# Optimization experiments

Hardware: AMD Instinct MI355X
Metric: run time of the kernel (lower is better)

The kernel has to match this reference:

```python
import jax, jax.numpy as jnp
import numpy as np

FREQ_DIM = 32
TIME_DIM = 32
HEADS = 8
TWO_PI = 6.283185307179586


def get_embeddings(B, H, W, freq_dim, time_dim, dtype):
    # freq embeddings over the height (frequency) axis
    nf = freq_dim // 2
    ln_x = jnp.log2(jnp.arange(0, H * nf, dtype=jnp.float32))
    ln_x = ln_x.at[0].set(-2.0)
    ln_x = ln_x.reshape(H, nf).T  # [nf, H]
    ln_x = ln_x * jnp.arange(1, nf + 1, dtype=jnp.float32)[:, None]
    # view_as_real(exp(1j*theta)) -> (cos, sin), interleaved per order along channel dim
    freq = jnp.stack([jnp.cos(ln_x), jnp.sin(ln_x)], axis=1).reshape(freq_dim, H)  # [freq_dim, H]
    freq = jnp.broadcast_to(freq[None, :, :, None], (B, freq_dim, H, W))

    # time embeddings over the width (time) axis
    nt = time_dim // 2
    k = jnp.arange(0, nt, dtype=jnp.float32) + 0.5  # [nt]
    x = jnp.arange(0, nt * W, dtype=jnp.float32).reshape(W, nt).T  # [nt, W]
    theta = k[:, None] * x / (W * nt) * TWO_PI  # [nt, W]
    time = jnp.stack([jnp.cos(theta), jnp.sin(theta)], axis=1).reshape(time_dim, W)  # [time_dim, W]
    time = jnp.broadcast_to(time[None, :, None, :], (B, time_dim, H, W))

    return jnp.concatenate([freq, time], axis=1).astype(dtype)  # [B, freq_dim+time_dim, H, W]


def setup_inputs() -> dict:
    key = jax.random.key(0)
    ks = jax.random.split(key, 6)
    B, C, H, W = 2, 512, 64, 32
    qkC = C + FREQ_DIM + TIME_DIM  # 576
    inner = HEADS * 64  # 512
    return {
        "hidden_states": jax.random.normal(ks[0], (B, C, H, W), dtype=jnp.float32),
        "Wq": jax.random.normal(ks[1], (qkC, inner), dtype=jnp.float32) * 0.02,
        "Wk": jax.random.normal(ks[2], (qkC, inner), dtype=jnp.float32) * 0.02,
        "Wv": jax.random.normal(ks[3], (C, inner), dtype=jnp.float32) * 0.02,
        "Wout": jax.random.normal(ks[4], (inner, C), dtype=jnp.float32) * 0.02,
        "bout": jnp.zeros((C,), dtype=jnp.float32),
    }


def reference(hidden_states, Wq, Wk, Wv, Wout, bout):
    B, C, H, W = hidden_states.shape
    emb = get_embeddings(B, H, W, FREQ_DIM, TIME_DIM, hidden_states.dtype)
    qk_hs = jnp.concatenate([hidden_states, emb], axis=1)  # [B, qkC, H, W]

    S = H * W
    qk_hs = qk_hs.reshape(B, -1, S).transpose(0, 2, 1)  # [B, S, qkC]
    v_hs = hidden_states.reshape(B, C, S).transpose(0, 2, 1)  # [B, S, C]

    q = qk_hs @ Wq  # [B, S, inner]
    k = qk_hs @ Wk
    v = v_hs @ Wv

    hd_qk = q.shape[-1] // HEADS
    hd_v = v.shape[-1] // HEADS
    q = q.reshape(B, S, HEADS, hd_qk).transpose(0, 2, 1, 3)  # [B, h, S, d]
    k = k.reshape(B, S, HEADS, hd_qk).transpose(0, 2, 1, 3)
    v = v.reshape(B, S, HEADS, hd_v).transpose(0, 2, 1, 3)

    scale = 1.0 / jnp.sqrt(jnp.asarray(hd_qk, dtype=q.dtype))
    scores = jnp.einsum('bhqd,bhkd->bhqk', q, k) * scale
    attn = jax.nn.softmax(scores, axis=-1)
    o = jnp.einsum('bhqk,bhkd->bhqd', attn, v)  # [B, h, S, d_v]

    o = o.transpose(0, 2, 1, 3).reshape(B, S, HEADS * hd_v)
    o = o @ Wout + bout  # [B, S, C]
    o = o.transpose(0, 2, 1).reshape(B, C, H, W)

    return o + hidden_states  # residual_connection=True, rescale_output_factor=1.0
```

## Files before the change

kernel.cpp:

```cpp
#include <hip/hip_runtime.h>
#include <math.h>

#define B_    2
#define C_    512
#define H_    64
#define W_    32
#define S_    2048
#define QKC_  576
#define INNER_ 512
#define NH_   8
#define HD_   64
#define TWO_PI_ 6.283185307179586f

typedef __attribute__((ext_vector_type(8))) short bfrag;
typedef __attribute__((ext_vector_type(4))) float ffrag;
typedef __attribute__((ext_vector_type(16))) float f16v;

typedef __attribute__((address_space(1))) const unsigned int as1_u32;
typedef __attribute__((address_space(3))) unsigned int as3_u32;

__device__ __forceinline__ ushort f2bf(float f) {
    unsigned u = __builtin_bit_cast(unsigned, f);
    unsigned r = (u + 0x7FFFu + ((u >> 16) & 1u)) >> 16;
    return (ushort)r;
}

__device__ __forceinline__ f16v zero16() {
    f16v z;
    #pragma unroll
    for (int i = 0; i < 16; i++) z[i] = 0.f;
    return z;
}

#define GLD(gp_, lp_) __builtin_amdgcn_global_load_lds((as1_u32*)(gp_), (as3_u32*)(lp_), 16, 0, 0)
#define EXPA(dst_, x_) asm("v_exp_f32 %0, %1" : "=v"(dst_) : "v"(x_))
#define SC_LOG2E 0.18033688011f

__global__ void k_trans_emb(const float* __restrict__ hid, ushort* __restrict__ X) {
    __shared__ float t[32][33];
    int b  = blockIdx.z;
    int s0 = blockIdx.x * 32, c0 = blockIdx.y * 32;
    int tx = threadIdx.x, ty = threadIdx.y;
    if (c0 < 512) {
        t[ty][tx] = hid[((size_t)b * C_ + (c0 + ty)) * S_ + s0 + tx];
        __syncthreads();
        X[((size_t)(b * S_ + s0 + ty)) * QKC_ + c0 + tx] = f2bf(t[tx][ty]);
    } else {
        int c = c0 - 512 + tx;
        int s = s0 + ty;
        int h = s >> 5, w = s & 31;
        float val;
        if (c < 32) {
            int f = c >> 1;
            int n = h * 16 + f;
            float lx = (n == 0) ? -2.0f : log2f((float)n);
            float arg = lx * (float)(f + 1);
            val = (c & 1) ? sinf(arg) : cosf(arg);
        } else {
            int tt = (c - 32) >> 1;
            float theta = ((float)tt + 0.5f) * (float)(w * 16 + tt) * (TWO_PI_ / 512.0f);
            val = (c & 1) ? sinf(theta) : cosf(theta);
        }
        X[(size_t)(b * S_ + s) * QKC_ + c0 + tx] = f2bf(val);
    }
}

__global__ void k_wtrans_all(const float* __restrict__ Wq, const float* __restrict__ Wk,
                             const float* __restrict__ Wv, const float* __restrict__ Wo,
                             ushort* __restrict__ Wqt, ushort* __restrict__ Wkt,
                             ushort* __restrict__ Wvt, ushort* __restrict__ Wot) {
    __shared__ float t[32][33];
    int z = blockIdx.z;
    const float* W; ushort* Wt; int K;
    if (z == 0)      { W = Wq; Wt = Wqt; K = QKC_; }
    else if (z == 1) { W = Wk; Wt = Wkt; K = QKC_; }
    else if (z == 2) { W = Wv; Wt = Wvt; K = C_; }
    else             { W = Wo; Wt = Wot; K = INNER_; }
    int k0 = blockIdx.x * 32, n0 = blockIdx.y * 32;
    if (k0 >= K) return;
    int tx = threadIdx.x, ty = threadIdx.y;
    t[ty][tx] = W[(size_t)(k0 + ty) * 512 + n0 + tx];
    __syncthreads();
    Wt[(size_t)(n0 + ty) * K + k0 + tx] = f2bf(t[tx][ty]);
}

#define GSTAGE(buf_, k0_) {                                                   \
    _Pragma("unroll")                                                         \
    for (int i_ = 0; i_ < 6; i_++)                                            \
        GLD(gp[i_] + (k0_), tl + (buf_) * 12288 + lo[i_]); }

__global__ __launch_bounds__(256, 3) void k_qkv(const ushort* __restrict__ X,
                                                const ushort* __restrict__ Wqt,
                                                const ushort* __restrict__ Wkt,
                                                const ushort* __restrict__ Wvt,
                                                ushort* __restrict__ Qb,
                                                ushort* __restrict__ Kpk,
                                                ushort* __restrict__ Vpk) {
    __shared__ ushort __attribute__((aligned(16))) tl[2 * 12288];

    int tid = threadIdx.x;
    int l = tid & 63, wv = tid >> 6;
    int wr = wv >> 1, wc = wv & 1;
    int bid = blockIdx.x;
    int lgc = (bid & 7) * 96 + (bid >> 3);
    int bx = lgc % 24, by = lgc / 24;
    int n0 = bx * 64, m0 = by * 128;
    int sel = n0 >> 9, n0l = n0 & 511;
    const ushort* Bt = (sel == 0) ? Wqt : (sel == 1) ? Wkt : Wvt;
    const int K = (sel < 2) ? QKC_ : C_;
    const int nst = K >> 6;
    int l15 = l & 15, lg = l >> 4;
    int swz = l15 & 7;

    const ushort* gp[6];
    unsigned lo[6];
    {
        int rsub = l >> 3;
        int clog = (l & 7) ^ rsub;
        #pragma unroll
        for (int i = 0; i < 6; i++) {
            int c = wv * 6 + i;
            lo[i] = c * 512;
            if (c < 16) gp[i] = X  + (size_t)(m0  + c * 8        + rsub) * QKC_ + clog * 8;
            else        gp[i] = Bt + (size_t)(n0l + (c - 16) * 8 + rsub) * K    + clog * 8;
        }
    }

    ffrag acc[4][2];
    #pragma unroll
    for (int i = 0; i < 4; i++)
        #pragma unroll
        for (int j = 0; j < 2; j++) acc[i][j] = (ffrag){0.f, 0.f, 0.f, 0.f};

    GSTAGE(0, 0);
    int cur = 0;
    for (int kt = 0; kt < nst; kt++) {
        __syncthreads();
        if (kt + 1 < nst) GSTAGE(cur ^ 1, (kt + 1) * 64);
        const ushort* As = tl + cur * 12288;
        const ushort* Bs = As + 8192;
        #pragma unroll
        for (int ks = 0; ks < 2; ks++) {
            int cl = ks * 4 + lg;
            int ch = (cl ^ swz) * 8;
            bfrag af[4], bf[2];
            #pragma unroll
            for (int mi = 0; mi < 4; mi++)
                af[mi] = *(const bfrag*)(As + (wr * 64 + mi * 16 + l15) * 64 + ch);
            #pragma unroll
            for (int nj = 0; nj < 2; nj++)
                bf[nj] = *(const bfrag*)(Bs + (wc * 32 + nj * 16 + l15) * 64 + ch);
            #pragma unroll
            for (int mi = 0; mi < 4; mi++)
                #pragma unroll
                for (int nj = 0; nj < 2; nj++)
                    acc[mi][nj] = __builtin_amdgcn_mfma_f32_16x16x32_bf16(af[mi], bf[nj], acc[mi][nj], 0, 0, 0);
        }
        cur ^= 1;
    }

    if (sel == 0) {
        #pragma unroll
        for (int mi = 0; mi < 4; mi++)
            #pragma unroll
            for (int nj = 0; nj < 2; nj++)
                #pragma unroll
                for (int r = 0; r < 4; r++) {
                    int row = m0 + wr * 64 + mi * 16 + lg * 4 + r;
                    int col = n0l + wc * 32 + nj * 16 + l15;
                    Qb[(size_t)row * INNER_ + col] = f2bf(acc[mi][nj][r]);
                }
    } else {
        ushort (*Ct)[136] = (ushort(*)[136])tl;
        __syncthreads();
        #pragma unroll
        for (int mi = 0; mi < 4; mi++)
            #pragma unroll
            for (int nj = 0; nj < 2; nj++)
                #pragma unroll
                for (int r = 0; r < 4; r++)
                    Ct[wc * 32 + nj * 16 + l15][wr * 64 + mi * 16 + lg * 4 + r] = f2bf(acc[mi][nj][r]);
        __syncthreads();
        int pair = (m0 >> 11) * 8 + (n0l >> 6);
        int kvb0 = (m0 & 2047) >> 5;
        if (sel == 1) {
            #pragma unroll
            for (int p = 0; p < 4; p++) {
                int cid = tid + p * 256;
                int sl = cid >> 7, kv = cid & 127;
                bfrag tmp;
                #pragma unroll
                for (int j = 0; j < 8; j++) tmp[j] = (short)Ct[sl * 8 + j][kv];
                ushort* dst = Kpk + ((size_t)((pair * 64 + kvb0 + (kv >> 5)) * 8 + sl)) * 256 + (kv & 31) * 8;
                *(uint4*)dst = __builtin_bit_cast(uint4, tmp);
            }
        } else {
            #pragma unroll
            for (int p = 0; p < 4; p++) {
                int cid = tid + p * 256;
                int d = cid >> 4, mc = cid & 15;
                uint4 v = *(uint4*)&Ct[d][mc * 8];
                ushort* dst = Vpk + ((size_t)((pair * 64 + kvb0 + (mc >> 2)) * 4 + (mc & 3))) * 512 + d * 8;
                *(uint4*)dst = v;
            }
        }
    }
}

__global__ __launch_bounds__(256, 2) void k_og(const ushort* __restrict__ Ob,
                                               const ushort* __restrict__ Wot,
                                               const float* __restrict__ bias,
                                               const float* __restrict__ hid,
                                               float* __restrict__ out) {
    __shared__ ushort __attribute__((aligned(16))) tl[2 * 12288];

    int tid = threadIdx.x;
    int l = tid & 63, wv = tid >> 6;
    int wr = wv >> 1, wc = wv & 1;
    int bid = blockIdx.x;
    int lgc = (bid & 7) * 32 + (bid >> 3);
    int bx = lgc & 7, by = lgc >> 3;
    int n0 = bx * 64, m0 = by * 128;
    int l15 = l & 15, lg = l >> 4;
    int swz = l15 & 7;

    const ushort* gp[6];
    unsigned lo[6];
    {
        int rsub = l >> 3;
        int clog = (l & 7) ^ rsub;
        #pragma unroll
        for (int i = 0; i < 6; i++) {
            int c = wv * 6 + i;
            lo[i] = c * 512;
            if (c < 16) gp[i] = Ob  + (size_t)(m0 + c * 8        + rsub) * INNER_ + clog * 8;
            else        gp[i] = Wot + (size_t)(n0 + (c - 16) * 8 + rsub) * INNER_ + clog * 8;
        }
    }

    ffrag acc[4][2];
    #pragma unroll
    for (int i = 0; i < 4; i++)
        #pragma unroll
        for (int j = 0; j < 2; j++) acc[i][j] = (ffrag){0.f, 0.f, 0.f, 0.f};

    GSTAGE(0, 0);
    int cur = 0;
    for (int kt = 0; kt < 8; kt++) {
        __syncthreads();
        if (kt < 7) GSTAGE(cur ^ 1, (kt + 1) * 64);
        const ushort* As = tl + cur * 12288;
        const ushort* Bs = As + 8192;
        #pragma unroll
        for (int ks = 0; ks < 2; ks++) {
            int cl = ks * 4 + lg;
            int ch = (cl ^ swz) * 8;
            bfrag af[4], bf[2];
            #pragma unroll
            for (int mi = 0; mi < 4; mi++)
                af[mi] = *(const bfrag*)(As + (wr * 64 + mi * 16 + l15) * 64 + ch);
            #pragma unroll
            for (int nj = 0; nj < 2; nj++)
                bf[nj] = *(const bfrag*)(Bs + (wc * 32 + nj * 16 + l15) * 64 + ch);
            #pragma unroll
            for (int mi = 0; mi < 4; mi++)
                #pragma unroll
                for (int nj = 0; nj < 2; nj++)
                    acc[mi][nj] = __builtin_amdgcn_mfma_f32_16x16x32_bf16(af[mi], bf[nj], acc[mi][nj], 0, 0, 0);
        }
        cur ^= 1;
    }

    float (*Cf)[129] = (float(*)[129])tl;
    float bv[2];
    #pragma unroll
    for (int nj = 0; nj < 2; nj++) bv[nj] = bias[n0 + wc * 32 + nj * 16 + l15];
    __syncthreads();
    #pragma unroll
    for (int mi = 0; mi < 4; mi++)
        #pragma unroll
        for (int nj = 0; nj < 2; nj++)
            #pragma unroll
            for (int r = 0; r < 4; r++)
                Cf[wc * 32 + nj * 16 + l15][wr * 64 + mi * 16 + lg * 4 + r] = acc[mi][nj][r] + bv[nj];
    __syncthreads();
    int b = m0 >> 11, s0m = m0 & 2047;
    #pragma unroll
    for (int p = 0; p < 8; p++) {
        int f = p * 256 + tid;
        int c = f >> 5, sq = (f & 31) * 4;
        size_t o = (((size_t)(b * 512 + n0 + c)) << 11) + s0m + sq;
        float4 hv = *(const float4*)(hid + o);
        float4 cv = *(float4*)&Cf[c][sq];
        cv.x += hv.x; cv.y += hv.y; cv.z += hv.z; cv.w += hv.w;
        *(float4*)(out + o) = cv;
    }
}

#define CVTPK(dst, a, b) asm("v_cvt_pk_bf16_f32 %0, %1, %2" : "=v"(dst) : "v"(a), "v"(b))
#define SWAP32(a, b)     asm("v_permlane32_swap_b32 %0, %1" : "+v"(a), "+v"(b))

#define KLOAD(dst_, kt_) {                                                    \
    const ushort* g_ = kpb + (size_t)(kt_) * 2048 + kro;                      \
    _Pragma("unroll")                                                         \
    for (int ks_ = 0; ks_ < 4; ks_++) dst_[ks_] = *(const bfrag*)(g_ + ks_ * 512); }

#define VLOAD(dst_, kt_) {                                                    \
    const ushort* g_ = vpb + (size_t)(kt_) * 2048 + vro;                      \
    dst_[0] = *(const bfrag*)(g_);                                            \
    dst_[1] = *(const bfrag*)(g_ + 256);                                      \
    dst_[2] = *(const bfrag*)(g_ + 1024);                                     \
    dst_[3] = *(const bfrag*)(g_ + 1280); }

#define ABODY(kf_, vf_, a0_, a1_) {                                           \
    f16v sf = zero16();                                                       \
    __builtin_amdgcn_s_setprio(1);                                            \
    sf = __builtin_amdgcn_mfma_f32_32x32x16_bf16(kf_[0], qf[0], sf, 0, 0, 0); \
    sf = __builtin_amdgcn_mfma_f32_32x32x16_bf16(kf_[1], qf[1], sf, 0, 0, 0); \
    sf = __builtin_amdgcn_mfma_f32_32x32x16_bf16(kf_[2], qf[2], sf, 0, 0, 0); \
    sf = __builtin_amdgcn_mfma_f32_32x32x16_bf16(kf_[3], qf[3], sf, 0, 0, 0); \
    __builtin_amdgcn_s_setprio(0);                                            \
    float ls0 = 0.f, ls1 = 0.f, ls2 = 0.f, ls3 = 0.f;                         \
    _Pragma("unroll")                                                         \
    for (int j = 0; j < 4; j++) {                                             \
        float p0; EXPA(p0, sf[j]      * SC_LOG2E);                            \
        float p1; EXPA(p1, sf[j + 4]  * SC_LOG2E);                            \
        float p2; EXPA(p2, sf[j + 8]  * SC_LOG2E);                            \
        float p3; EXPA(p3, sf[j + 12] * SC_LOG2E);                            \
        sf[j] = p0; sf[j + 4] = p1; sf[j + 8] = p2; sf[j + 12] = p3;          \
        ls0 += p0; ls1 += p1; ls2 += p2; ls3 += p3;                           \
    }                                                                         \
    l_run += (ls0 + ls1) + (ls2 + ls3);                                       \
    __builtin_amdgcn_s_setprio(1);                                            \
    _Pragma("unroll")                                                         \
    for (int s = 0; s < 2; s++) {                                             \
        unsigned A0, B0, A1, B1;                                              \
        CVTPK(A0, sf[s * 8 + 0], sf[s * 8 + 1]); CVTPK(B0, sf[s * 8 + 4], sf[s * 8 + 5]); \
        SWAP32(A0, B0);                                                       \
        CVTPK(A1, sf[s * 8 + 2], sf[s * 8 + 3]); CVTPK(B1, sf[s * 8 + 6], sf[s * 8 + 7]); \
        SWAP32(A1, B1);                                                       \
        uint4 u_; u_.x = A0; u_.y = A1; u_.z = B0; u_.w = B1;                 \
        bfrag pa_ = __builtin_bit_cast(bfrag, u_);                            \
        a0_ = __builtin_amdgcn_mfma_f32_32x32x16_bf16(vf_[s * 2],     pa_, a0_, 0, 0, 0); \
        a1_ = __builtin_amdgcn_mfma_f32_32x32x16_bf16(vf_[s * 2 + 1], pa_, a1_, 0, 0, 0); \
    }                                                                         \
    __builtin_amdgcn_s_setprio(0); }

__global__ __launch_bounds__(512, 2) void k_attn(const ushort* __restrict__ Qf,
                                                 const ushort* __restrict__ Kpk,
                                                 const ushort* __restrict__ Vpk,
                                                 ushort* __restrict__ Ob) {
    __shared__ __attribute__((aligned(16))) char smem[68608];
    float* cmb = (float*)smem;
    float* lsh = (float*)(smem + 67584);

    const int id  = blockIdx.x;
    const int xcd = id & 7, wi = id >> 3;
    const int pair = xcd * 2 + (wi >> 4);
    const int qt   = wi & 15;
    const int hd = pair & 7, b = pair >> 3;

    const int tid = threadIdx.x;
    const int l = tid & 63, wvid = tid >> 6;
    const int qi = wvid >> 1, sp = wvid & 1;
    const int l31 = l & 31, hi = l >> 5;
    const int hoff = hd * HD_;
    const int brow = b * S_ + qt * 128;

    bfrag qf[4];
    {
        const ushort* qp = Qf + (size_t)(brow + qi * 32 + l31) * INNER_ + hoff + hi * 8;
        #pragma unroll
        for (int ks = 0; ks < 4; ks++) qf[ks] = *(const bfrag*)(qp + ks * 16);
    }

    const ushort* kpb = Kpk + ((size_t)pair * 64 + sp * 32) * 2048;
    const ushort* vpb = Vpk + ((size_t)pair * 64 + sp * 32) * 2048;
    const int kro = hi * 256 + l31 * 8;
    const int vro = hi * 512 + l31 * 8;

    float l_run = 0.f;
    f16v acc0a = zero16(), acc1a = zero16();
    f16v acc0b = zero16(), acc1b = zero16();

    bfrag kc[4], vc[4], kn[4], vn[4];
    KLOAD(kc, 0); VLOAD(vc, 0);

    for (int it = 0; it < 32; it += 2) {
        if (it + 1 < 32) { KLOAD(kn, it + 1); VLOAD(vn, it + 1); }
        ABODY(kc, vc, acc0a, acc1a);
        if (it + 2 < 32) { KLOAD(kc, it + 2); VLOAD(vc, it + 2); }
        ABODY(kn, vn, acc0b, acc1b);
    }

    f16v acc0 = acc0a, acc1 = acc1a;
    #pragma unroll
    for (int j = 0; j < 16; j++) { acc0[j] += acc0b[j]; acc1[j] += acc1b[j]; }
    l_run += __shfl_xor(l_run, 32);

    if (hi == 0) lsh[wvid * 32 + l31] = l_run;
    {
        float* creg = cmb + wvid * 2112;
        #pragma unroll
        for (int j = 0; j < 16; j++) {
            int d0 = (j & 3) + 8 * (j >> 2) + 4 * hi;
            creg[d0 * 33 + l31]        = acc0[j];
            creg[(d0 + 32) * 33 + l31] = acc1[j];
        }
    }
    __syncthreads();
    #pragma unroll
    for (int p2 = 0; p2 < 2; p2++) {
        int f = p2 * 512 + tid;
        int qg4 = f >> 8;
        int t2 = f & 255;
        int qq = t2 >> 3, cc = t2 & 7;
        float lt = lsh[(qg4 * 2) * 32 + qq] + lsh[(qg4 * 2 + 1) * 32 + qq];
        float inv = 1.0f / lt;
        bfrag ov;
        #pragma unroll
        for (int j = 0; j < 8; j++) {
            int d = cc * 8 + j;
            float s = cmb[(qg4 * 2) * 2112 + d * 33 + qq] + cmb[(qg4 * 2 + 1) * 2112 + d * 33 + qq];
            ov[j] = (short)f2bf(s * inv);
        }
        *(uint4*)(Ob + (size_t)(brow + qg4 * 32 + qq) * INNER_ + hoff + cc * 8) = __builtin_bit_cast(uint4, ov);
    }
}

extern "C" void kernel_launch(void* const* d_in, const int* in_sizes, int n_in,
                              void* d_out, int out_size, void* d_ws, size_t ws_size,
                              hipStream_t stream) {
    const float* hid  = (const float*)d_in[0];
    const float* Wq   = (const float*)d_in[1];
    const float* Wk   = (const float*)d_in[2];
    const float* Wv   = (const float*)d_in[3];
    const float* Wout = (const float*)d_in[4];
    const float* bout = (const float*)d_in[5];
    float* out = (float*)d_out;

    const int M = B_ * S_;
    char* w = (char*)d_ws;
    ushort* X    = (ushort*)w;                    w += (size_t)M * QKC_ * 2;
    ushort* Qb   = (ushort*)w;                    w += (size_t)M * INNER_ * 2;
    ushort* Kpk  = (ushort*)w;                    w += (size_t)M * INNER_ * 2;
    ushort* Vpk  = (ushort*)w;                    w += (size_t)M * INNER_ * 2;
    ushort* Ob   = (ushort*)w;                    w += (size_t)M * INNER_ * 2;
    ushort* Wqt  = (ushort*)w;                    w += (size_t)INNER_ * QKC_ * 2;
    ushort* Wkt  = (ushort*)w;                    w += (size_t)INNER_ * QKC_ * 2;
    ushort* Wvt  = (ushort*)w;                    w += (size_t)INNER_ * C_ * 2;
    ushort* Wot  = (ushort*)w;                    w += (size_t)C_ * INNER_ * 2;

    k_wtrans_all<<<dim3(18, 16, 4), dim3(32, 32), 0, stream>>>(Wq, Wk, Wv, Wout,
                                                               Wqt, Wkt, Wvt, Wot);
    k_trans_emb<<<dim3(S_ / 32, 18, B_), dim3(32, 32), 0, stream>>>(hid, X);

    k_qkv<<<dim3(768), 256, 0, stream>>>(X, Wqt, Wkt, Wvt, Qb, Kpk, Vpk);

    k_attn<<<dim3(256), 512, 0, stream>>>(Qb, Kpk, Vpk, Ob);

    k_og<<<dim3(256), 256, 0, stream>>>(Ob, Wot, bout, hid, out);
}
```

Before: 60.81 us.

## Let each attention wave process two query tiles per K/V load and split keys four ways

```diff
diff --git a/kernel.cpp b/kernel.cpp
--- a/kernel.cpp
+++ b/kernel.cpp
@@ -168,7 +168,7 @@
                 for (int r = 0; r < 4; r++) {
                     int row = m0 + wr * 64 + mi * 16 + lg * 4 + r;
                     int col = n0l + wc * 32 + nj * 16 + l15;
-                    Qb[(size_t)row * INNER_ + col] = f2bf(acc[mi][nj][r]);
+                    Qb[(size_t)row * INNER_ + col] = f2bf(acc[mi][nj][r] * SC_LOG2E);
                 }
     } else {
         ushort (*Ct)[136] = (ushort(*)[136])tl;
@@ -312,47 +312,48 @@
     dst_[2] = *(const bfrag*)(g_ + 1024);                                     \
     dst_[3] = *(const bfrag*)(g_ + 1280); }
 
-#define ABODY(kf_, vf_, a0_, a1_) {                                           \
-    f16v sf = zero16();                                                       \
-    __builtin_amdgcn_s_setprio(1);                                            \
-    sf = __builtin_amdgcn_mfma_f32_32x32x16_bf16(kf_[0], qf[0], sf, 0, 0, 0); \
-    sf = __builtin_amdgcn_mfma_f32_32x32x16_bf16(kf_[1], qf[1], sf, 0, 0, 0); \
-    sf = __builtin_amdgcn_mfma_f32_32x32x16_bf16(kf_[2], qf[2], sf, 0, 0, 0); \
-    sf = __builtin_amdgcn_mfma_f32_32x32x16_bf16(kf_[3], qf[3], sf, 0, 0, 0); \
-    __builtin_amdgcn_s_setprio(0);                                            \
-    float ls0 = 0.f, ls1 = 0.f, ls2 = 0.f, ls3 = 0.f;                         \
-    _Pragma("unroll")                                                         \
-    for (int j = 0; j < 4; j++) {                                             \
-        float p0; EXPA(p0, sf[j]      * SC_LOG2E);                            \
-        float p1; EXPA(p1, sf[j + 4]  * SC_LOG2E);                            \
-        float p2; EXPA(p2, sf[j + 8]  * SC_LOG2E);                            \
-        float p3; EXPA(p3, sf[j + 12] * SC_LOG2E);                            \
-        sf[j] = p0; sf[j + 4] = p1; sf[j + 8] = p2; sf[j + 12] = p3;          \
-        ls0 += p0; ls1 += p1; ls2 += p2; ls3 += p3;                           \
-    }                                                                         \
-    l_run += (ls0 + ls1) + (ls2 + ls3);                                       \
-    __builtin_amdgcn_s_setprio(1);                                            \
+#define PVHALF(sf_, vf_, a0_, a1_) {                                          \
     _Pragma("unroll")                                                         \
     for (int s = 0; s < 2; s++) {                                             \
         unsigned A0, B0, A1, B1;                                              \
-        CVTPK(A0, sf[s * 8 + 0], sf[s * 8 + 1]); CVTPK(B0, sf[s * 8 + 4], sf[s * 8 + 5]); \
+        CVTPK(A0, sf_[s * 8 + 0], sf_[s * 8 + 1]); CVTPK(B0, sf_[s * 8 + 4], sf_[s * 8 + 5]); \
         SWAP32(A0, B0);                                                       \
-        CVTPK(A1, sf[s * 8 + 2], sf[s * 8 + 3]); CVTPK(B1, sf[s * 8 + 6], sf[s * 8 + 7]); \
+        CVTPK(A1, sf_[s * 8 + 2], sf_[s * 8 + 3]); CVTPK(B1, sf_[s * 8 + 6], sf_[s * 8 + 7]); \
         SWAP32(A1, B1);                                                       \
         uint4 u_; u_.x = A0; u_.y = A1; u_.z = B0; u_.w = B1;                 \
         bfrag pa_ = __builtin_bit_cast(bfrag, u_);                            \
         a0_ = __builtin_amdgcn_mfma_f32_32x32x16_bf16(vf_[s * 2],     pa_, a0_, 0, 0, 0); \
         a1_ = __builtin_amdgcn_mfma_f32_32x32x16_bf16(vf_[s * 2 + 1], pa_, a1_, 0, 0, 0); \
+    } }
+
+#define ABODY(kf_, vf_) {                                                     \
+    f16v sfA = zero16(), sfB = zero16();                                      \
+    __builtin_amdgcn_s_setprio(1);                                            \
+    _Pragma("unroll")                                                         \
+    for (int ks = 0; ks < 4; ks++) {                                          \
+        sfA = __builtin_amdgcn_mfma_f32_32x32x16_bf16(kf_[ks], qfA[ks], sfA, 0, 0, 0); \
+        sfB = __builtin_amdgcn_mfma_f32_32x32x16_bf16(kf_[ks], qfB[ks], sfB, 0, 0, 0); \
     }                                                                         \
+    __builtin_amdgcn_s_setprio(0);                                            \
+    float lsA = 0.f, lsB = 0.f;                                               \
+    _Pragma("unroll")                                                         \
+    for (int j = 0; j < 16; j++) {                                            \
+        float pA; EXPA(pA, sfA[j]); sfA[j] = pA; lsA += pA;                   \
+        float pB; EXPA(pB, sfB[j]); sfB[j] = pB; lsB += pB;                   \
+    }                                                                         \
+    lA += lsA; lB += lsB;                                                     \
+    __builtin_amdgcn_s_setprio(1);                                            \
+    PVHALF(sfA, vf_, accA0, accA1);                                           \
+    PVHALF(sfB, vf_, accB0, accB1);                                           \
     __builtin_amdgcn_s_setprio(0); }
 
 __global__ __launch_bounds__(512, 2) void k_attn(const ushort* __restrict__ Qf,
                                                  const ushort* __restrict__ Kpk,
                                                  const ushort* __restrict__ Vpk,
                                                  ushort* __restrict__ Ob) {
-    __shared__ __attribute__((aligned(16))) char smem[68608];
+    __shared__ __attribute__((aligned(16))) char smem[35840];
     float* cmb = (float*)smem;
-    float* lsh = (float*)(smem + 67584);
+    float* lsh = (float*)(smem + 33792);
 
     const int id  = blockIdx.x;
     const int xcd = id & 7, wi = id >> 3;
@@ -362,69 +363,87 @@
 
     const int tid = threadIdx.x;
     const int l = tid & 63, wvid = tid >> 6;
-    const int qi = wvid >> 1, sp = wvid & 1;
+    const int qi = wvid >> 2, sp = wvid & 3;
     const int l31 = l & 31, hi = l >> 5;
     const int hoff = hd * HD_;
     const int brow = b * S_ + qt * 128;
 
-    bfrag qf[4];
+    bfrag qfA[4], qfB[4];
     {
-        const ushort* qp = Qf + (size_t)(brow + qi * 32 + l31) * INNER_ + hoff + hi * 8;
-        #pragma unroll
-        for (int ks = 0; ks < 4; ks++) qf[ks] = *(const bfrag*)(qp + ks * 16);
-    }
-
-    const ushort* kpb = Kpk + ((size_t)pair * 64 + sp * 32) * 2048;
-    const ushort* vpb = Vpk + ((size_t)pair * 64 + sp * 32) * 2048;
+        const ushort* qpA = Qf + (size_t)(brow + qi * 64 + l31) * INNER_ + hoff + hi * 8;
+        const ushort* qpB = qpA + (size_t)32 * INNER_;
+        #pragma unroll
+        for (int ks = 0; ks < 4; ks++) {
+            qfA[ks] = *(const bfrag*)(qpA + ks * 16);
+            qfB[ks] = *(const bfrag*)(qpB + ks * 16);
+        }
+    }
+
+    const ushort* kpb = Kpk + ((size_t)pair * 64 + sp * 16) * 2048;
+    const ushort* vpb = Vpk + ((size_t)pair * 64 + sp * 16) * 2048;
     const int kro = hi * 256 + l31 * 8;
     const int vro = hi * 512 + l31 * 8;
 
-    float l_run = 0.f;
-    f16v acc0a = zero16(), acc1a = zero16();
-    f16v acc0b = zero16(), acc1b = zero16();
+    float lA = 0.f, lB = 0.f;
+    f16v accA0 = zero16(), accA1 = zero16();
+    f16v accB0 = zero16(), accB1 = zero16();
 
     bfrag kc[4], vc[4], kn[4], vn[4];
     KLOAD(kc, 0); VLOAD(vc, 0);
 
-    for (int it = 0; it < 32; it += 2) {
-        if (it + 1 < 32) { KLOAD(kn, it + 1); VLOAD(vn, it + 1); }
-        ABODY(kc, vc, acc0a, acc1a);
-        if (it + 2 < 32) { KLOAD(kc, it + 2); VLOAD(vc, it + 2); }
-        ABODY(kn, vn, acc0b, acc1b);
-    }
-
-    f16v acc0 = acc0a, acc1 = acc1a;
-    #pragma unroll
-    for (int j = 0; j < 16; j++) { acc0[j] += acc0b[j]; acc1[j] += acc1b[j]; }
-    l_run += __shfl_xor(l_run, 32);
-
-    if (hi == 0) lsh[wvid * 32 + l31] = l_run;
-    {
-        float* creg = cmb + wvid * 2112;
-        #pragma unroll
-        for (int j = 0; j < 16; j++) {
-            int d0 = (j & 3) + 8 * (j >> 2) + 4 * hi;
-            creg[d0 * 33 + l31]        = acc0[j];
-            creg[(d0 + 32) * 33 + l31] = acc1[j];
-        }
-    }
-    __syncthreads();
+    for (int it = 0; it < 16; it += 2) {
+        if (it + 1 < 16) { KLOAD(kn, it + 1); VLOAD(vn, it + 1); }
+        ABODY(kc, vc);
+        if (it + 2 < 16) { KLOAD(kc, it + 2); VLOAD(vc, it + 2); }
+        ABODY(kn, vn);
+    }
+
+    lA += __shfl_xor(lA, 32);
+    lB += __shfl_xor(lB, 32);
+
+    if (hi == 0) {
+        lsh[((qi * 2 + 0) * 4 + sp) * 32 + l31] = lA;
+        lsh[((qi * 2 + 1) * 4 + sp) * 32 + l31] = lB;
+    }
+    #pragma unroll
+    for (int p = 0; p < 4; p++) {
+        if (sp == p) {
+            float* cA = cmb + (qi * 2 + 0) * 2112;
+            float* cB = cmb + (qi * 2 + 1) * 2112;
+            #pragma unroll
+            for (int j = 0; j < 16; j++) {
+                int d0 = (j & 3) + 8 * (j >> 2) + 4 * hi;
+                if (p == 0) {
+                    cA[d0 * 33 + l31]        = accA0[j];
+                    cA[(d0 + 32) * 33 + l31] = accA1[j];
+                    cB[d0 * 33 + l31]        = accB0[j];
+                    cB[(d0 + 32) * 33 + l31] = accB1[j];
+                } else {
+                    cA[d0 * 33 + l31]        += accA0[j];
+                    cA[(d0 + 32) * 33 + l31] += accA1[j];
+                    cB[d0 * 33 + l31]        += accB0[j];
+                    cB[(d0 + 32) * 33 + l31] += accB1[j];
+                }
+            }
+        }
+        __syncthreads();
+    }
     #pragma unroll
     for (int p2 = 0; p2 < 2; p2++) {
         int f = p2 * 512 + tid;
-        int qg4 = f >> 8;
+        int qig = f >> 8;
         int t2 = f & 255;
         int qq = t2 >> 3, cc = t2 & 7;
-        float lt = lsh[(qg4 * 2) * 32 + qq] + lsh[(qg4 * 2 + 1) * 32 + qq];
+        float lt = lsh[(qig * 4 + 0) * 32 + qq] + lsh[(qig * 4 + 1) * 32 + qq]
+                 + lsh[(qig * 4 + 2) * 32 + qq] + lsh[(qig * 4 + 3) * 32 + qq];
         float inv = 1.0f / lt;
         bfrag ov;
         #pragma unroll
         for (int j = 0; j < 8; j++) {
             int d = cc * 8 + j;
-            float s = cmb[(qg4 * 2) * 2112 + d * 33 + qq] + cmb[(qg4 * 2 + 1) * 2112 + d * 33 + qq];
-            ov[j] = (short)f2bf(s * inv);
-        }
-        *(uint4*)(Ob + (size_t)(brow + qg4 * 32 + qq) * INNER_ + hoff + cc * 8) = __builtin_bit_cast(uint4, ov);
+            ov[j] = (short)f2bf(cmb[qig * 2112 + d * 33 + qq] * inv);
+        }
+        *(uint4*)(Ob + (size_t)(brow + qig * 32 + qq) * INNER_ + hoff + cc * 8) = __builtin_bit_cast(uint4, ov);
     }
 }
 
```

After: 59.81 us. About the same (-1.6%).
